# Kernel tuning notes

Measured on AMD Instinct MI355X. Metric: run time of the kernel, lower is better.

The kernel has to match this reference:

```python
import jax, jax.numpy as jnp
import numpy as np

ALPHA = 0.2          # leaky_relu negative slope
NEG_INF = -9e15      # mask fill value (matches torch source)


def setup_inputs() -> dict:
    key = jax.random.key(0)
    k_h, k_mask, k_W, k_a = jax.random.split(key, 4)
    B, N, F_in, F_out = 4, 65536, 128, 128
    h = jax.random.normal(k_h, (B, N, F_in), dtype=jnp.float32)
    # op_mask > 0 means "mask out this neighbor" (prev/self/next)
    op_mask = jax.random.randint(k_mask, (B, N, 3), 0, 2, dtype=jnp.int32)
    # xavier_uniform-style init for params
    lim_W = 1.414 * np.sqrt(6.0 / (F_in + F_out))
    W = jax.random.uniform(k_W, (F_in, F_out), dtype=jnp.float32, minval=-lim_W, maxval=lim_W)
    lim_a = 1.414 * np.sqrt(6.0 / (2 * F_out + 1))
    a = jax.random.uniform(k_a, (2 * F_out, 1), dtype=jnp.float32, minval=-lim_a, maxval=lim_a)
    return {"h": h, "op_mask": op_mask, "W": W, "a": a}


def reference(h, op_mask, W, a):
    F_out = W.shape[1]
    Wh = jnp.matmul(h, W)                                   # [B, N, F]
    # windowed neighbors: prev (roll +1), self, next (roll -1)
    Wh_concat = jnp.stack(
        [jnp.roll(Wh, 1, axis=1), Wh, jnp.roll(Wh, -1, axis=1)], axis=-2
    )                                                       # [B, N, 3, F]
    Wh1 = jnp.matmul(Wh, a[:F_out])                         # [B, N, 1]
    Wh2 = jnp.matmul(Wh, a[F_out:])                         # [B, N, 1]
    Wh2_concat = jnp.stack(
        [jnp.roll(Wh2, 1, axis=1), Wh2, jnp.roll(Wh2, -1, axis=1)], axis=-1
    )                                                       # [B, N, 1, 3]
    e = jax.nn.leaky_relu(Wh1[..., None] + Wh2_concat, ALPHA)  # [B, N, 1, 3]
    e = jnp.where(op_mask[:, :, None, :] > 0, jnp.float32(NEG_INF), e)
    attention = jax.nn.softmax(e, axis=-1)                  # [B, N, 1, 3]
    # dropout_prob = 0.0 (eval-equivalent), so dropout is identity
    h_new = jnp.matmul(attention, Wh_concat).squeeze(-2)    # [B, N, F]
    return h_new
```

## Files before the change

kernel.cpp:

```cpp
#include <hip/hip_runtime.h>
#include <hip/hip_bf16.h>

typedef __attribute__((ext_vector_type(8))) short short8;
typedef __attribute__((ext_vector_type(4))) float f32x4;

#define ALPHA 0.2f
#define NEG_INF -9e15f
#define QB 14
#define NB 4
#define NN 65536
#define TPB 4682
#define TTOT (TPB * NB)
#define NBLK 512
#define WPB 8
#define NWAVES (NBLK * WPB)

__device__ __forceinline__ short fb(float x) {
    __hip_bfloat16 b = __float2bfloat16(x);
    return __builtin_bit_cast(short, b);
}
__device__ __forceinline__ float bf2f(unsigned short x) {
    union { unsigned int u; float f; } v; v.u = ((unsigned int)x) << 16;
    return v.f;
}

__global__ __launch_bounds__(256) void prep_w(const float* __restrict__ W,
                                              const float* __restrict__ a,
                                              unsigned short* __restrict__ ws) {
    const int t = threadIdx.x;
    if (blockIdx.x < 8) {
        int qg = blockIdx.x * 256 + t;
        int lane = qg & 63, f = qg >> 6;
        int kk = f >> 3, ni = f & 7;
        int slot = kk * 9 + ni;
        int n = ni * 16 + (lane & 15);
        int k0 = kk * 32 + ((lane >> 4) & 3) * 8;
        short8 o;
        #pragma unroll
        for (int j = 0; j < 8; ++j) o[j] = fb(W[(k0 + j) * 128 + n]);
        *(short8*)(ws + (size_t)(slot * 64 + lane) * 8) = o;
    } else {
        __shared__ float wa[2][128];
        {
            int k = t >> 1, sel = t & 1;
            const f32x4* wr4 = (const f32x4*)(W + k * 128);
            const f32x4* av4 = (const f32x4*)(a + sel * 128);
            float s = 0.f;
            #pragma unroll
            for (int c4 = 0; c4 < 32; ++c4) {
                f32x4 wv = wr4[c4], av = av4[c4];
                s += wv[0]*av[0] + wv[1]*av[1] + wv[2]*av[2] + wv[3]*av[3];
            }
            wa[sel][k] = s;
        }
        __syncthreads();
        {
            int lane = t & 63, kk = t >> 6;
            int l15 = lane & 15, lg = (lane >> 4) & 3;
            int k0 = kk * 32 + lg * 8;
            int slot = kk * 9 + 8;
            short8 o;
            #pragma unroll
            for (int j = 0; j < 8; ++j) o[j] = fb((l15 < 2) ? wa[l15][k0 + j] : 0.f);
            *(short8*)(ws + (size_t)(slot * 64 + lane) * 8) = o;
        }
    }
}

__global__ __launch_bounds__(512)
void gat_fused(const float* __restrict__ h, const int* __restrict__ opm,
               const unsigned short* __restrict__ ws, float* __restrict__ out) {
    __shared__ __align__(16) char Btab[36864];
    __shared__ __align__(16) char strip[WPB][4096];
    __shared__ float whs[WPB][32];
    __shared__ int   msk[WPB][44];

    const int t = threadIdx.x;
    const int lane = t & 63;
    const int w = t >> 6;
    const int l15 = lane & 15;
    const int lg = (lane >> 4) & 3;

    #pragma unroll
    for (int i = 0; i < 5; ++i) {
        int idx = t + i * 512;
        if (idx < 2304) ((f32x4*)Btab)[idx] = ((const f32x4*)ws)[idx];
    }
    __syncthreads();
    const short8* Bt = (const short8*)Btab;
    char* st = strip[w];

    f32x4 al[4][2];
    int mreg = 0;
    {
        int wt = blockIdx.x * WPB + w;
        if (wt < TTOT) {
            int b = wt / TPB;
            int tt = wt - b * TPB;
            int out0 = tt * QB;
            int g = out0 - 1 + l15;
            if (g < 0) g += NN; else if (g >= NN) g -= NN;
            const char* rp = (const char*)(h + (size_t)b * NN * 128) +
                             (size_t)g * 512 + (lg << 5);
            #pragma unroll
            for (int kk = 0; kk < 4; ++kk) {
                al[kk][0] = *(const f32x4*)(rp + (kk << 7));
                al[kk][1] = *(const f32x4*)(rp + (kk << 7) + 16);
            }
            if (lane < 42) {
                int mi_ = out0 * 3 + lane;
                if (mi_ > NN * 3 - 1) mi_ = NN * 3 - 1;
                mreg = opm[(size_t)b * (NN * 3) + mi_];
            }
        }
    }

    for (int wt = blockIdx.x * WPB + w; wt < TTOT; wt += NWAVES) {
        const int b = wt / TPB;
        const int tt = wt - b * TPB;
        const int out0 = tt * QB;
        const int orows = min(QB, NN - out0);
        float* outB = out + (size_t)b * NN * 128;

        short8 av[4];
        #pragma unroll
        for (int kk = 0; kk < 4; ++kk) {
            av[kk][0] = fb(al[kk][0][0]); av[kk][1] = fb(al[kk][0][1]);
            av[kk][2] = fb(al[kk][0][2]); av[kk][3] = fb(al[kk][0][3]);
            av[kk][4] = fb(al[kk][1][0]); av[kk][5] = fb(al[kk][1][1]);
            av[kk][6] = fb(al[kk][1][2]); av[kk][7] = fb(al[kk][1][3]);
        }
        if (lane < 42) msk[w][lane] = mreg;

        const int wt2 = wt + NWAVES;
        if (wt2 < TTOT) {
            int b2 = wt2 / TPB;
            int tt2 = wt2 - b2 * TPB;
            int out02 = tt2 * QB;
            int g2 = out02 - 1 + l15;
            if (g2 < 0) g2 += NN; else if (g2 >= NN) g2 -= NN;
            const char* rp2 = (const char*)(h + (size_t)b2 * NN * 128) +
                              (size_t)g2 * 512 + (lg << 5);
            #pragma unroll
            for (int kk = 0; kk < 4; ++kk) {
                al[kk][0] = *(const f32x4*)(rp2 + (kk << 7));
                al[kk][1] = *(const f32x4*)(rp2 + (kk << 7) + 16);
            }
            if (lane < 42) {
                int mi_ = out02 * 3 + lane;
                if (mi_ > NN * 3 - 1) mi_ = NN * 3 - 1;
                mreg = opm[(size_t)b2 * (NN * 3) + mi_];
            }
        }
        __builtin_amdgcn_sched_barrier(0);

        f32x4 acc[8];
        f32x4 acc2 = (f32x4){0.f, 0.f, 0.f, 0.f};
        #pragma unroll
        for (int ni = 0; ni < 8; ++ni) acc[ni] = (f32x4){0.f, 0.f, 0.f, 0.f};
        #pragma unroll
        for (int kk = 0; kk < 4; ++kk) {
            #pragma unroll
            for (int ni = 0; ni < 8; ++ni)
                acc[ni] = __builtin_amdgcn_mfma_f32_16x16x32_bf16(
                    av[kk], Bt[(kk * 9 + ni) * 64 + lane], acc[ni], 0, 0, 0);
            acc2 = __builtin_amdgcn_mfma_f32_16x16x32_bf16(
                av[kk], Bt[(kk * 9 + 8) * 64 + lane], acc2, 0, 0, 0);
        }

        #pragma unroll
        for (int ni = 0; ni < 8; ++ni) {
            int col = (ni << 4) + l15;
            #pragma unroll
            for (int j = 0; j < 4; ++j) {
                int row = (lg << 2) + j;
                *(unsigned short*)(st + row * 256 + ((col << 1) ^ ((row & 4) << 4))) =
                    (unsigned short)fb(acc[ni][j]);
            }
        }
        if (l15 < 2) {
            #pragma unroll
            for (int j = 0; j < 4; ++j)
                whs[w][((lg << 2) + j) * 2 + l15] = acc2[j];
        }

        #pragma unroll
        for (int it = 0; it < 7; ++it) {
            int rr = (it << 1) + (lane >> 5);
            if (rr >= orows) continue;
            int r = rr + 1;
            int mk0 = msk[w][rr * 3];
            int mk1 = msk[w][rr * 3 + 1];
            int mk2 = msk[w][rr * 3 + 2];
            float w1 = whs[w][r * 2];
            float e0 = w1 + whs[w][(r - 1) * 2 + 1];
            float e1 = w1 + whs[w][r * 2 + 1];
            float e2 = w1 + whs[w][(r + 1) * 2 + 1];
            e0 = e0 > 0.f ? e0 : ALPHA * e0;
            e1 = e1 > 0.f ? e1 : ALPHA * e1;
            e2 = e2 > 0.f ? e2 : ALPHA * e2;
            if (mk0 > 0) e0 = NEG_INF;
            if (mk1 > 0) e1 = NEG_INF;
            if (mk2 > 0) e2 = NEG_INF;
            float m = fmaxf(e0, fmaxf(e1, e2));
            float x0 = __expf(e0 - m), x1 = __expf(e1 - m), x2 = __expf(e2 - m);
            float inv = 1.f / (x0 + x1 + x2);
            float a0 = x0 * inv, a1 = x1 * inv, a2 = x2 * inv;
            int cb = (lane & 31) << 3;
            ushort4 wm = *(const ushort4*)(st + (r - 1) * 256 + (cb ^ (((r - 1) & 4) << 4)));
            ushort4 w0 = *(const ushort4*)(st + r * 256 + (cb ^ ((r & 4) << 4)));
            ushort4 wp = *(const ushort4*)(st + (r + 1) * 256 + (cb ^ (((r + 1) & 4) << 4)));
            f32x4 res;
            res[0] = a0 * bf2f(wm.x) + a1 * bf2f(w0.x) + a2 * bf2f(wp.x);
            res[1] = a0 * bf2f(wm.y) + a1 * bf2f(w0.y) + a2 * bf2f(wp.y);
            res[2] = a0 * bf2f(wm.z) + a1 * bf2f(w0.z) + a2 * bf2f(wp.z);
            res[3] = a0 * bf2f(wm.w) + a1 * bf2f(w0.w) + a2 * bf2f(wp.w);
            *(f32x4*)(outB + (size_t)(out0 + rr) * 128 + ((lane & 31) << 2)) = res;
        }
    }
}

extern "C" void kernel_launch(void* const* d_in, const int* in_sizes, int n_in,
                              void* d_out, int out_size, void* d_ws, size_t ws_size,
                              hipStream_t stream) {
    const float* h   = (const float*)d_in[0];
    const int*   opm = (const int*)d_in[1];
    const float* W   = (const float*)d_in[2];
    const float* a   = (const float*)d_in[3];
    float* out = (float*)d_out;
    unsigned short* ws = (unsigned short*)d_ws;
    prep_w<<<9, 256, 0, stream>>>(W, a, ws);
    gat_fused<<<NBLK, 512, 0, stream>>>(h, opm, ws, out);
}
```

Measured before the change: 60.85 us.

## Transpose MFMA operands and combine neighbors via cross-lane shuffles instead of LDS

Swaps the MFMA A/B operands so each lane's accumulator holds one row's features across columns. Neighbor rows and the attention logits then come from wave shuffles instead of a bf16 LDS staging strip. Each lane now loads its own row's three mask values directly rather than going through shared memory. This drops the LDS round trip and the bf16 rounding of Wh in the combine step, at the cost of many ds_bpermute shuffles (two per accumulator element) and less coalesced 16-byte output stores.

```diff
diff --git a/kernel.cpp b/kernel.cpp
--- a/kernel.cpp
+++ b/kernel.cpp
@@ -18,10 +18,6 @@
 __device__ __forceinline__ short fb(float x) {
     __hip_bfloat16 b = __float2bfloat16(x);
     return __builtin_bit_cast(short, b);
-}
-__device__ __forceinline__ float bf2f(unsigned short x) {
-    union { unsigned int u; float f; } v; v.u = ((unsigned int)x) << 16;
-    return v.f;
 }
 
 __global__ __launch_bounds__(256) void prep_w(const float* __restrict__ W,
@@ -71,9 +67,6 @@
 void gat_fused(const float* __restrict__ h, const int* __restrict__ opm,
                const unsigned short* __restrict__ ws, float* __restrict__ out) {
     __shared__ __align__(16) char Btab[36864];
-    __shared__ __align__(16) char strip[WPB][4096];
-    __shared__ float whs[WPB][32];
-    __shared__ int   msk[WPB][44];
 
     const int t = threadIdx.x;
     const int lane = t & 63;
@@ -88,10 +81,9 @@
     }
     __syncthreads();
     const short8* Bt = (const short8*)Btab;
-    char* st = strip[w];
 
     f32x4 al[4][2];
-    int mreg = 0;
+    int mr0 = 0, mr1 = 0, mr2 = 0;
     {
         int wt = blockIdx.x * WPB + w;
         if (wt < TTOT) {
@@ -107,11 +99,10 @@
                 al[kk][0] = *(const f32x4*)(rp + (kk << 7));
                 al[kk][1] = *(const f32x4*)(rp + (kk << 7) + 16);
             }
-            if (lane < 42) {
-                int mi_ = out0 * 3 + lane;
-                if (mi_ > NN * 3 - 1) mi_ = NN * 3 - 1;
-                mreg = opm[(size_t)b * (NN * 3) + mi_];
-            }
+            int gm = out0 + l15 - 1;
+            if (gm < 0) gm = 0; else if (gm >= NN) gm = NN - 1;
+            const int* mp = opm + ((size_t)b * NN + gm) * 3;
+            mr0 = mp[0]; mr1 = mp[1]; mr2 = mp[2];
         }
     }
 
@@ -130,7 +121,7 @@
             av[kk][4] = fb(al[kk][1][0]); av[kk][5] = fb(al[kk][1][1]);
             av[kk][6] = fb(al[kk][1][2]); av[kk][7] = fb(al[kk][1][3]);
         }
-        if (lane < 42) msk[w][lane] = mreg;
+        const int mk0 = mr0, mk1 = mr1, mk2 = mr2;
 
         const int wt2 = wt + NWAVES;
         if (wt2 < TTOT) {
@@ -146,11 +137,10 @@
                 al[kk][0] = *(const f32x4*)(rp2 + (kk << 7));
                 al[kk][1] = *(const f32x4*)(rp2 + (kk << 7) + 16);
             }
-            if (lane < 42) {
-                int mi_ = out02 * 3 + lane;
-                if (mi_ > NN * 3 - 1) mi_ = NN * 3 - 1;
-                mreg = opm[(size_t)b2 * (NN * 3) + mi_];
-            }
+            int gm2 = out02 + l15 - 1;
+            if (gm2 < 0) gm2 = 0; else if (gm2 >= NN) gm2 = NN - 1;
+            const int* mp2 = opm + ((size_t)b2 * NN + gm2) * 3;
+            mr0 = mp2[0]; mr1 = mp2[1]; mr2 = mp2[2];
         }
         __builtin_amdgcn_sched_barrier(0);
 
@@ -163,59 +153,44 @@
             #pragma unroll
             for (int ni = 0; ni < 8; ++ni)
                 acc[ni] = __builtin_amdgcn_mfma_f32_16x16x32_bf16(
-                    av[kk], Bt[(kk * 9 + ni) * 64 + lane], acc[ni], 0, 0, 0);
+                    Bt[(kk * 9 + ni) * 64 + lane], av[kk], acc[ni], 0, 0, 0);
             acc2 = __builtin_amdgcn_mfma_f32_16x16x32_bf16(
-                av[kk], Bt[(kk * 9 + 8) * 64 + lane], acc2, 0, 0, 0);
-        }
-
+                Bt[(kk * 9 + 8) * 64 + lane], av[kk], acc2, 0, 0, 0);
+        }
+
+        float wh1 = __shfl(acc2[0], l15);
+        float w2c = __shfl(acc2[1], l15);
+        float w2m = __shfl(acc2[1], (l15 + 15) & 15);
+        float w2p = __shfl(acc2[1], (l15 + 1) & 15);
+
+        float e0 = wh1 + w2m;
+        float e1 = wh1 + w2c;
+        float e2 = wh1 + w2p;
+        e0 = e0 > 0.f ? e0 : ALPHA * e0;
+        e1 = e1 > 0.f ? e1 : ALPHA * e1;
+        e2 = e2 > 0.f ? e2 : ALPHA * e2;
+        if (mk0 > 0) e0 = NEG_INF;
+        if (mk1 > 0) e1 = NEG_INF;
+        if (mk2 > 0) e2 = NEG_INF;
+        float m = fmaxf(e0, fmaxf(e1, e2));
+        float x0 = __expf(e0 - m), x1 = __expf(e1 - m), x2 = __expf(e2 - m);
+        float inv = 1.f / (x0 + x1 + x2);
+        float a0 = x0 * inv, a1 = x1 * inv, a2 = x2 * inv;
+
+        const int lm = (lane & 48) | ((l15 + 15) & 15);
+        const int lp = (lane & 48) | ((l15 + 1) & 15);
+        const bool doS = (l15 >= 1) && (l15 <= orows);
+        float* orow = outB + (size_t)(out0 + l15 - 1) * 128 + (lg << 2);
         #pragma unroll
         for (int ni = 0; ni < 8; ++ni) {
-            int col = (ni << 4) + l15;
+            f32x4 res;
             #pragma unroll
             for (int j = 0; j < 4; ++j) {
-                int row = (lg << 2) + j;
-                *(unsigned short*)(st + row * 256 + ((col << 1) ^ ((row & 4) << 4))) =
-                    (unsigned short)fb(acc[ni][j]);
-            }
-        }
-        if (l15 < 2) {
-            #pragma unroll
-            for (int j = 0; j < 4; ++j)
-                whs[w][((lg << 2) + j) * 2 + l15] = acc2[j];
-        }
-
-        #pragma unroll
-        for (int it = 0; it < 7; ++it) {
-            int rr = (it << 1) + (lane >> 5);
-            if (rr >= orows) continue;
-            int r = rr + 1;
-            int mk0 = msk[w][rr * 3];
-            int mk1 = msk[w][rr * 3 + 1];
-            int mk2 = msk[w][rr * 3 + 2];
-            float w1 = whs[w][r * 2];
-            float e0 = w1 + whs[w][(r - 1) * 2 + 1];
-            float e1 = w1 + whs[w][r * 2 + 1];
-            float e2 = w1 + whs[w][(r + 1) * 2 + 1];
-            e0 = e0 > 0.f ? e0 : ALPHA * e0;
-            e1 = e1 > 0.f ? e1 : ALPHA * e1;
-            e2 = e2 > 0.f ? e2 : ALPHA * e2;
-            if (mk0 > 0) e0 = NEG_INF;
-            if (mk1 > 0) e1 = NEG_INF;
-            if (mk2 > 0) e2 = NEG_INF;
-            float m = fmaxf(e0, fmaxf(e1, e2));
-            float x0 = __expf(e0 - m), x1 = __expf(e1 - m), x2 = __expf(e2 - m);
-            float inv = 1.f / (x0 + x1 + x2);
-            float a0 = x0 * inv, a1 = x1 * inv, a2 = x2 * inv;
-            int cb = (lane & 31) << 3;
-            ushort4 wm = *(const ushort4*)(st + (r - 1) * 256 + (cb ^ (((r - 1) & 4) << 4)));
-            ushort4 w0 = *(const ushort4*)(st + r * 256 + (cb ^ ((r & 4) << 4)));
-            ushort4 wp = *(const ushort4*)(st + (r + 1) * 256 + (cb ^ (((r + 1) & 4) << 4)));
-            f32x4 res;
-            res[0] = a0 * bf2f(wm.x) + a1 * bf2f(w0.x) + a2 * bf2f(wp.x);
-            res[1] = a0 * bf2f(wm.y) + a1 * bf2f(w0.y) + a2 * bf2f(wp.y);
-            res[2] = a0 * bf2f(wm.z) + a1 * bf2f(w0.z) + a2 * bf2f(wp.z);
-            res[3] = a0 * bf2f(wm.w) + a1 * bf2f(w0.w) + a2 * bf2f(wp.w);
-            *(f32x4*)(outB + (size_t)(out0 + rr) * 128 + ((lane & 31) << 2)) = res;
+                float wmv = __shfl(acc[ni][j], lm);
+                float wpv = __shfl(acc[ni][j], lp);
+                res[j] = a0 * wmv + a1 * acc[ni][j] + a2 * wpv;
+            }
+            if (doS) *(f32x4*)(orow + (ni << 4)) = res;
         }
     }
 }
```

After: 70.35 us. 15.6% more time.
